# Performance work log

Measured on AMD Instinct MI355X. Metric: run time of the kernel, lower is better.

Reference implementation:

```python
import jax, jax.numpy as jnp
import numpy as np

B, L, DIM, H = 1, 2048, 3072, 24
D = DIM // H  # 128
EPS = 1e-6

def setup_inputs() -> dict:
    key = jax.random.key(0)
    ks = jax.random.split(key, 7)
    x = jax.random.normal(ks[0], (B, L, DIM), dtype=jnp.float32)
    pe = jax.random.normal(ks[1], (B, 1, L, D // 2, 2, 2), dtype=jnp.float32)
    w_qkv = jax.random.normal(ks[2], (DIM, 3 * DIM), dtype=jnp.float32) / np.sqrt(DIM)
    q_scale = jnp.ones((D,), dtype=jnp.float32)
    k_scale = jnp.ones((D,), dtype=jnp.float32)
    w_proj = jax.random.normal(ks[3], (DIM, DIM), dtype=jnp.float32) / np.sqrt(DIM)
    b_proj = jnp.zeros((DIM,), dtype=jnp.float32)
    return {"x": x, "pe": pe, "w_qkv": w_qkv, "q_scale": q_scale,
            "k_scale": k_scale, "w_proj": w_proj, "b_proj": b_proj}

def _rmsnorm(t, scale):
    # flax nn.RMSNorm: t * rsqrt(mean(t^2, -1) + eps) * scale
    ms = jnp.mean(jnp.square(t), axis=-1, keepdims=True)
    return t * jax.lax.rsqrt(ms + EPS) * scale

def _apply_rope(xq, xk, pe):
    # xq/xk: [B,H,L,D]; pe: [B,1,L,D/2,2,2]
    xq_ = xq.reshape(*xq.shape[:-1], -1, 1, 2)
    xk_ = xk.reshape(*xk.shape[:-1], -1, 1, 2)
    xq_out = pe[..., 0] * xq_[..., 0] + pe[..., 1] * xq_[..., 1]
    xk_out = pe[..., 0] * xk_[..., 0] + pe[..., 1] * xk_[..., 1]
    return xq_out.reshape(xq.shape), xk_out.reshape(xk.shape)

def reference(x, pe, w_qkv, q_scale, k_scale, w_proj, b_proj):
    qkv = jnp.einsum('bld,de->ble', x, w_qkv)            # [B,L,3*DIM]
    qkv = qkv.reshape(B, L, 3, H, D)
    qkv = jnp.moveaxis(qkv, 2, 0)                          # [3,B,H?,..]
    q, k, v = jnp.transpose(qkv, (0, 1, 3, 2, 4))          # each [B,H,L,D]
    q = _rmsnorm(q, q_scale).astype(v.dtype)
    k = _rmsnorm(k, k_scale).astype(v.dtype)
    q, k = _apply_rope(q, k, pe)
    scale = 1.0 / np.sqrt(D)
    scores = jnp.einsum('bhqd,bhkd->bhqk', q, k) * scale   # [B,H,L,L]
    attn = jax.nn.softmax(scores, axis=-1)
    out = jnp.einsum('bhqk,bhkd->bhqd', attn, v)           # [B,H,L,D]
    out = jnp.transpose(out, (0, 2, 1, 3)).reshape(B, L, DIM)
    return jnp.einsum('bld,de->ble', out, w_proj) + b_proj
```

## Files before the change

kernel.cpp:

```cpp
#include <hip/hip_runtime.h>

#define L_    2048
#define DIM_  3072
#define H_    24
#define D_    128
#define NQKV  9216

typedef __attribute__((ext_vector_type(8))) short bf16x8;
typedef __attribute__((ext_vector_type(4))) short bf16x4;
typedef __attribute__((ext_vector_type(4))) float f32x4;

__device__ __forceinline__ unsigned short f2bf(float f) {
  union { float f; unsigned u; } v; v.f = f;
  unsigned r = v.u + 0x7fffu + ((v.u >> 16) & 1u);
  return (unsigned short)(r >> 16);
}

__device__ __forceinline__ void gload_lds16(const void* g, void* l) {
  auto* lp = reinterpret_cast<__attribute__((address_space(3))) unsigned int*>(
      reinterpret_cast<uintptr_t>(l));
  auto* gp = reinterpret_cast<const __attribute__((address_space(1))) unsigned int*>(
      reinterpret_cast<uintptr_t>(g));
  __builtin_amdgcn_global_load_lds(gp, lp, 16, 0, 0);
}

__global__ __launch_bounds__(256)
void castAll(const float* __restrict__ x,  unsigned short* __restrict__ xb,
             const float* __restrict__ w0, unsigned short* __restrict__ o0,
             const float* __restrict__ w1, unsigned short* __restrict__ o1) {
  const int K = 3072;
  const int by = blockIdx.y;
  if (by >= 192) {
    int blk = (by - 192) * 24 + blockIdx.x;
    int total = (L_ * DIM_) >> 2;
    int stride = 2304 * 256;
    for (int i = blk * 256 + threadIdx.x; i < total; i += stride) {
      float4 v = ((const float4*)x)[i];
      ushort4 o;
      o.x = f2bf(v.x); o.y = f2bf(v.y); o.z = f2bf(v.z); o.w = f2bf(v.w);
      ((ushort4*)xb)[i] = o;
    }
    return;
  }
  const float* in; unsigned short* out; int N, n0;
  if (by < 144) { in = w0; out = o0; N = 9216; n0 = by * 64; }
  else          { in = w1; out = o1; N = 3072; n0 = (by - 144) * 64; }
  const int tid  = threadIdx.x;
  const int lane = tid & 63;
  const int wave = tid >> 6;
  const int nq = lane & 7;
  const int kq = lane >> 3;
  const int k0 = blockIdx.x * 128 + (wave & 1) * 64 + kq * 8;
  const int nb = n0 + (wave >> 1) * 32 + nq * 4;
  float4 v[8];
  #pragma unroll
  for (int i = 0; i < 8; i++)
    v[i] = *(const float4*)&in[(size_t)(k0 + i) * N + nb];
  #pragma unroll
  for (int j = 0; j < 4; j++) {
    bf16x8 o;
    #pragma unroll
    for (int i = 0; i < 8; i++)
      o[i] = (short)f2bf(((const float*)&v[i])[j]);
    *(bf16x8*)&out[(size_t)(nb + j) * K + k0] = o;
  }
}

__global__ __launch_bounds__(256, 3)
void gemm_qkv(const unsigned short* __restrict__ A,
              const unsigned short* __restrict__ Bt,
              const float* __restrict__ pe,
              const float* __restrict__ q_scale,
              const float* __restrict__ k_scale,
              unsigned short* __restrict__ Qo,
              unsigned short* __restrict__ Ko,
              unsigned short* __restrict__ Vt)
{
  const int K = DIM_;
  __shared__ __align__(16) unsigned short S[128 * 132];
  unsigned short* As = S;
  unsigned short* Bs = S + 128 * 64;
  const int tid  = threadIdx.x;
  const int wave = tid >> 6;
  const int lane = tid & 63;
  const int l15  = lane & 15;
  const int quad = lane >> 4;
  const int wm = wave >> 1, wn = wave & 1;

  const int lin = blockIdx.x;
  const int st  = lin >> 6;
  const int w6  = lin & 63;
  const int bn_idx = (st >> 1) * 8 + (w6 & 7);
  const int bm_idx = (st & 1) * 8 + (w6 >> 3);
  const int bm = bm_idx * 128;
  const int bn = bn_idx * 128;

  const int srow = lane >> 3;
  const int scol = (lane & 7) ^ srow;
  const unsigned short* Ag = A  + (size_t)(bm + wave * 32 + srow) * K + scol * 8;
  const unsigned short* Bg = Bt + (size_t)(bn + wave * 32 + srow) * K + scol * 8;
  unsigned short* Al = &As[(wave * 32) * 64];
  unsigned short* Bl = &Bs[(wave * 32) * 64];

  f32x4 acc[4][4];
  #pragma unroll
  for (int i = 0; i < 4; i++)
    #pragma unroll
    for (int j = 0; j < 4; j++) acc[i][j] = (f32x4){0.f, 0.f, 0.f, 0.f};

  for (int k0 = 0; k0 < K; k0 += 64) {
    __syncthreads();
    #pragma unroll
    for (int j = 0; j < 4; j++) {
      gload_lds16(Ag + (size_t)j * 8 * K + k0, Al + j * 8 * 64);
      gload_lds16(Bg + (size_t)j * 8 * K + k0, Bl + j * 8 * 64);
    }
    __syncthreads();
    #pragma unroll
    for (int ks = 0; ks < 2; ks++) {
      const int cph = ((ks * 4 + quad) ^ (l15 & 7)) * 8;
      bf16x8 af[4], bf[4];
      #pragma unroll
      for (int mt = 0; mt < 4; mt++)
        af[mt] = *(const bf16x8*)&As[(wm * 64 + mt * 16 + l15) * 64 + cph];
      #pragma unroll
      for (int nt = 0; nt < 4; nt++)
        bf[nt] = *(const bf16x8*)&Bs[(wn * 64 + nt * 16 + l15) * 64 + cph];
      #pragma unroll
      for (int mt = 0; mt < 4; mt++)
        #pragma unroll
        for (int nt = 0; nt < 4; nt++)
          acc[mt][nt] = __builtin_amdgcn_mfma_f32_16x16x32_bf16(
              af[mt], bf[nt], acc[mt][nt], 0, 0, 0);
    }
  }
  __syncthreads();

  if (bn_idx < 48) {
    const bool isQ = bn_idx < 24;
    const int  hh  = isQ ? bn_idx : bn_idx - 24;
    const float* sc = isQ ? q_scale : k_scale;
    unsigned short* dst = isQ ? Qo : Ko;
    float* rbuf = (float*)S;
    #pragma unroll
    for (int mt = 0; mt < 4; mt++)
      #pragma unroll
      for (int r = 0; r < 4; r++) {
        float p = 0.f;
        #pragma unroll
        for (int nt = 0; nt < 4; nt++) p += acc[mt][nt][r] * acc[mt][nt][r];
        p += __shfl_xor(p, 1); p += __shfl_xor(p, 2);
        p += __shfl_xor(p, 4); p += __shfl_xor(p, 8);
        if (l15 == 0) rbuf[wn * 128 + wm * 64 + mt * 16 + quad * 4 + r] = p;
      }
    __syncthreads();
    #pragma unroll
    for (int mt = 0; mt < 4; mt++)
      #pragma unroll
      for (int r = 0; r < 4; r++) {
        const int lrow = wm * 64 + mt * 16 + quad * 4 + r;
        const int lg = bm + lrow;
        float ms = (rbuf[lrow] + rbuf[128 + lrow]) * (1.f / 128.f);
        float rinv = rsqrtf(ms + 1e-6f);
        #pragma unroll
        for (int nt = 0; nt < 4; nt++) {
          const int d = wn * 64 + nt * 16 + l15;
          float n  = acc[mt][nt][r] * rinv * sc[d];
          float np = __shfl_xor(n, 1);
          float2 ab = *(const float2*)&pe[(size_t)lg * 256 + (d >> 1) * 4 + (d & 1) * 2];
          float xe = (d & 1) ? np : n;
          float xo = (d & 1) ? n  : np;
          float o = ab.x * xe + ab.y * xo;
          if (isQ) o *= (0.08838834764831845f * 1.4426950408889634f);
          dst[((size_t)hh * L_ + lg) * D_ + d] = f2bf(o);
        }
      }
  } else {
    const int hh = bn_idx - 48;
    unsigned short (*St)[132] = (unsigned short(*)[132])S;
    #pragma unroll
    for (int mt = 0; mt < 4; mt++)
      #pragma unroll
      for (int nt = 0; nt < 4; nt++)
        #pragma unroll
        for (int r = 0; r < 4; r++) {
          int row = wm * 64 + mt * 16 + quad * 4 + r;
          int col = wn * 64 + nt * 16 + l15;
          St[row][col] = f2bf(acc[mt][nt][r]);
        }
    __syncthreads();
    const int grp = tid >> 6;
    const int ll  = tid & 63;
    unsigned short* dstV = Vt + (size_t)hh * D_ * L_;
    #pragma unroll
    for (int dd = 0; dd < 32; dd += 4) {
      const int d = grp * 32 + dd;
      #pragma unroll
      for (int half = 0; half < 2; half++) {
        const int l = ll + half * 64;
        bf16x4 v4 = *(const bf16x4*)&St[l][d];
        #pragma unroll
        for (int j = 0; j < 4; j++)
          dstV[(size_t)(d + j) * L_ + bm + l] = ((const unsigned short*)&v4)[j];
      }
    }
  }
}

__global__ __launch_bounds__(256, 3)
void gemm_proj(const unsigned short* __restrict__ A,
               const unsigned short* __restrict__ Bt,
               const float* __restrict__ bias,
               float* __restrict__ out,
               int M, int N, int K)
{
  __shared__ unsigned short As[128 * 64];
  __shared__ unsigned short Bs[128 * 64];
  const int tid  = threadIdx.x;
  const int wave = tid >> 6;
  const int lane = tid & 63;
  const int l15  = lane & 15;
  const int quad = lane >> 4;
  const int wm = wave >> 1, wn = wave & 1;
  const int lin = blockIdx.x;
  const int st  = lin >> 6;
  const int w6  = lin & 63;
  const int bn = ((st >> 1) * 8 + (w6 & 7)) * 128;
  const int bm = ((st & 1) * 8 + (w6 >> 3)) * 128;

  const int srow = lane >> 3;
  const int scol = (lane & 7) ^ srow;
  const unsigned short* Ag = A  + (size_t)(bm + wave * 32 + srow) * K + scol * 8;
  const unsigned short* Bg = Bt + (size_t)(bn + wave * 32 + srow) * K + scol * 8;
  unsigned short* Al = &As[(wave * 32) * 64];
  unsigned short* Bl = &Bs[(wave * 32) * 64];

  f32x4 acc[4][4];
  #pragma unroll
  for (int i = 0; i < 4; i++)
    #pragma unroll
    for (int j = 0; j < 4; j++) acc[i][j] = (f32x4){0.f, 0.f, 0.f, 0.f};

  for (int k0 = 0; k0 < K; k0 += 64) {
    __syncthreads();
    #pragma unroll
    for (int j = 0; j < 4; j++) {
      gload_lds16(Ag + (size_t)j * 8 * K + k0, Al + j * 8 * 64);
      gload_lds16(Bg + (size_t)j * 8 * K + k0, Bl + j * 8 * 64);
    }
    __syncthreads();
    #pragma unroll
    for (int ks = 0; ks < 2; ks++) {
      const int cph = ((ks * 4 + quad) ^ (l15 & 7)) * 8;
      bf16x8 af[4], bf[4];
      #pragma unroll
      for (int mt = 0; mt < 4; mt++)
        af[mt] = *(const bf16x8*)&As[(wm * 64 + mt * 16 + l15) * 64 + cph];
      #pragma unroll
      for (int nt = 0; nt < 4; nt++)
        bf[nt] = *(const bf16x8*)&Bs[(wn * 64 + nt * 16 + l15) * 64 + cph];
      #pragma unroll
      for (int mt = 0; mt < 4; mt++)
        #pragma unroll
        for (int nt = 0; nt < 4; nt++)
          acc[mt][nt] = __builtin_amdgcn_mfma_f32_16x16x32_bf16(
              af[mt], bf[nt], acc[mt][nt], 0, 0, 0);
    }
  }
  float bcol[4];
  #pragma unroll
  for (int nt = 0; nt < 4; nt++)
    bcol[nt] = bias[bn + wn * 64 + nt * 16 + l15];
  #pragma unroll
  for (int mt = 0; mt < 4; mt++)
    #pragma unroll
    for (int nt = 0; nt < 4; nt++)
      #pragma unroll
      for (int r = 0; r < 4; r++) {
        int row = bm + wm * 64 + mt * 16 + quad * 4 + r;
        int col = bn + wn * 64 + nt * 16 + l15;
        out[(size_t)row * N + col] = acc[mt][nt][r] + bcol[nt];
      }
}

__global__ __launch_bounds__(256, 3)
void flash_attn(const unsigned short* __restrict__ Q,
                const unsigned short* __restrict__ K,
                const unsigned short* __restrict__ Vt,
                unsigned short* __restrict__ Out)
{
  __shared__ __align__(16) char smem[49152];
  float*  Obuf = (float*)smem;
  float2* mlb  = (float2*)(smem + 32768);
  float4* sAr  = (float4*)(smem + 33280);

  const int tid  = threadIdx.x;
  const int wave = tid >> 6;
  const int lane = tid & 63;
  const int l15  = lane & 15;
  const int quad = lane >> 4;
  const int qg = wave >> 1;
  const int kh = wave & 1;
  const int id   = blockIdx.x;
  const int slot = id >> 3;
  const int h    = (id & 7) * 3 + slot % 3;
  const int q0   = (slot / 3) * 64 + qg * 32;

  const unsigned short* Qh = Q  + (size_t)h * L_ * D_;
  const unsigned short* Kh = K  + (size_t)h * L_ * D_;
  const unsigned short* Vh = Vt + (size_t)h * D_ * L_;

  bf16x8 qf[2][4];
  #pragma unroll
  for (int nt = 0; nt < 2; nt++)
    #pragma unroll
    for (int kc = 0; kc < 4; kc++)
      qf[nt][kc] = *(const bf16x8*)&Qh[(size_t)(q0 + nt * 16 + l15) * D_ + kc * 32 + quad * 8];

  f32x4 oacc[2][8];
  #pragma unroll
  for (int i = 0; i < 2; i++)
    #pragma unroll
    for (int j = 0; j < 8; j++) oacc[i][j] = (f32x4){0.f, 0.f, 0.f, 0.f};
  float m_i[2] = {-1e30f, -1e30f}, l_i[2] = {0.f, 0.f};

  const int kr_l = lane >> 4;
  const int vr_l = lane >> 3;
  const int vcl  = (lane & 7) ^ vr_l;

  auto stageK = [&](int t, int b) {
    unsigned short* Ksb = (unsigned short*)(smem + b * 16384);
    #pragma unroll
    for (int ji = 0; ji < 4; ji++) {
      int Rr = wave * 16 + ji * 4;
      int cl = l15 ^ ((Rr + kr_l) & 15);
      gload_lds16(&Kh[(size_t)(t + Rr + kr_l) * D_ + cl * 8], &Ksb[Rr * 128]);
    }
  };
  auto stageV = [&](int t) {
    unsigned short* Vsb = (unsigned short*)(smem + 32768);
    #pragma unroll
    for (int ji = 0; ji < 4; ji++) {
      int R2 = wave * 32 + ji * 8;
      gload_lds16(&Vh[(size_t)(R2 + vr_l) * L_ + t + vcl * 8], &Vsb[R2 * 64]);
    }
  };

  stageK(0, 0);
  stageV(0);

  for (int t = 0; t < L_; t += 64) {
    const int cur = (t >> 6) & 1;
    const bool more = (t + 64 < L_);

    asm volatile("s_waitcnt vmcnt(4)" ::: "memory");
    __builtin_amdgcn_s_barrier();
    if (more) stageK(t + 64, cur ^ 1);

    const unsigned short* Ksc = (const unsigned short*)(smem + cur * 16384);
    const unsigned short* Vsc = (const unsigned short*)(smem + 32768);

    f32x4 s[2][2];
    #pragma unroll
    for (int i = 0; i < 2; i++)
      #pragma unroll
      for (int j = 0; j < 2; j++) s[i][j] = (f32x4){0.f, 0.f, 0.f, 0.f};
    __builtin_amdgcn_s_setprio(1);
    #pragma unroll
    for (int mt = 0; mt < 2; mt++) {
      const int krow = kh * 32 + mt * 16 + l15;
      #pragma unroll
      for (int kc = 0; kc < 4; kc++) {
        bf16x8 kf = *(const bf16x8*)&Ksc[krow * 128 + (((kc * 4 + quad) ^ l15) * 8)];
        s[mt][0] = __builtin_amdgcn_mfma_f32_16x16x32_bf16(kf, qf[0][kc], s[mt][0], 0, 0, 0);
        s[mt][1] = __builtin_amdgcn_mfma_f32_16x16x32_bf16(kf, qf[1][kc], s[mt][1], 0, 0, 0);
      }
    }
    __builtin_amdgcn_s_setprio(0);

    float vmax[2];
    #pragma unroll
    for (int nt = 0; nt < 2; nt++) {
      float a = fmaxf(fmaxf(s[0][nt][0], s[0][nt][1]), s[0][nt][2]);
      a = fmaxf(fmaxf(a, s[0][nt][3]), s[1][nt][0]);
      a = fmaxf(fmaxf(a, s[1][nt][1]), s[1][nt][2]);
      a = fmaxf(a, s[1][nt][3]);
      a = fmaxf(a, __shfl_xor(a, 16));
      vmax[nt] = fmaxf(a, __shfl_xor(a, 32));
    }
    if (!__all((vmax[0] - m_i[0] <= 11.5415603f) && (vmax[1] - m_i[1] <= 11.5415603f))) {
      float alpha[2];
      #pragma unroll
      for (int nt = 0; nt < 2; nt++) {
        float mnew = fmaxf(m_i[nt], vmax[nt]);
        alpha[nt] = exp2f(m_i[nt] - mnew);
        m_i[nt] = mnew;
        l_i[nt] *= alpha[nt];
      }
      float ar[2][4];
      #pragma unroll
      for (int qt = 0; qt < 2; qt++)
        #pragma unroll
        for (int r = 0; r < 4; r++)
          ar[qt][r] = __shfl(alpha[qt], quad * 4 + r);
      #pragma unroll
      for (int qt = 0; qt < 2; qt++)
        #pragma unroll
        for (int ntd = 0; ntd < 8; ntd++)
          #pragma unroll
          for (int r = 0; r < 4; r++)
            oacc[qt][ntd][r] *= ar[qt][r];
    }
    float rs[2] = {0.f, 0.f};
    #pragma unroll
    for (int mt = 0; mt < 2; mt++)
      #pragma unroll
      for (int nt = 0; nt < 2; nt++)
        #pragma unroll
        for (int r = 0; r < 4; r++) {
          float p = exp2f(s[mt][nt][r] - m_i[nt]);
          s[mt][nt][r] = p;
          rs[nt] += p;
        }
    #pragma unroll
    for (int nt = 0; nt < 2; nt++) {
      rs[nt] += __shfl_xor(rs[nt], 16);
      rs[nt] += __shfl_xor(rs[nt], 32);
      l_i[nt] += rs[nt];
    }
    bf16x4 pk[2][2];
    #pragma unroll
    for (int mt = 0; mt < 2; mt++)
      #pragma unroll
      for (int qt = 0; qt < 2; qt++) {
        union { unsigned int u2[2]; bf16x4 v4; } pku;
        asm("v_cvt_pk_bf16_f32 %0, %1, %2"
            : "=v"(pku.u2[0]) : "v"(s[mt][qt][0]), "v"(s[mt][qt][1]));
        asm("v_cvt_pk_bf16_f32 %0, %1, %2"
            : "=v"(pku.u2[1]) : "v"(s[mt][qt][2]), "v"(s[mt][qt][3]));
        pk[mt][qt] = pku.v4;
      }

    if (more) asm volatile("s_waitcnt vmcnt(4)" ::: "memory");
    else      asm volatile("s_waitcnt vmcnt(0)" ::: "memory");
    __builtin_amdgcn_s_barrier();

    __builtin_amdgcn_s_setprio(1);
    #pragma unroll
    for (int ntd = 0; ntd < 8; ntd++) {
      const int vrow = ntd * 16 + l15;
      #pragma unroll
      for (int mt = 0; mt < 2; mt++) {
        int phys = (kh * 4 + mt * 2 + (quad >> 1)) ^ (l15 & 7);
        bf16x4 vf = *(const bf16x4*)&Vsc[vrow * 64 + phys * 8 + (quad & 1) * 4];
        oacc[0][ntd] = __builtin_amdgcn_mfma_f32_16x16x16bf16_1k(pk[mt][0], vf, oacc[0][ntd], 0, 0, 0);
        oacc[1][ntd] = __builtin_amdgcn_mfma_f32_16x16x16bf16_1k(pk[mt][1], vf, oacc[1][ntd], 0, 0, 0);
      }
    }
    __builtin_amdgcn_s_setprio(0);

    if (more) {
      __builtin_amdgcn_s_barrier();
      stageV(t + 64);
    }
  }

  __syncthreads();
  if (kh == 1) {
    #pragma unroll
    for (int qt = 0; qt < 2; qt++)
      #pragma unroll
      for (int ntd = 0; ntd < 8; ntd++)
        #pragma unroll
        for (int r = 0; r < 4; r++)
          Obuf[(size_t)(qg * 32 + qt * 16 + quad * 4 + r) * 128 + ntd * 16 + l15] = oacc[qt][ntd][r];
    if (quad == 0)
      #pragma unroll
      for (int qt = 0; qt < 2; qt++)
        mlb[qg * 32 + qt * 16 + l15] = make_float2(m_i[qt], l_i[qt]);
  }
  __syncthreads();
  if (kh == 0 && quad == 0) {
    #pragma unroll
    for (int qt = 0; qt < 2; qt++) {
      float2 m1 = mlb[qg * 32 + qt * 16 + l15];
      float M  = fmaxf(m_i[qt], m1.x);
      float a0 = exp2f(m_i[qt] - M);
      float a1 = exp2f(m1.x - M);
      float Ls = l_i[qt] * a0 + m1.y * a1;
      sAr[qg * 32 + qt * 16 + l15] = make_float4(a0, a1, 1.f / Ls, 0.f);
    }
  }
  __syncthreads();
  if (kh == 0) {
    #pragma unroll
    for (int qt = 0; qt < 2; qt++)
      #pragma unroll
      for (int r = 0; r < 4; r++) {
        float4 A = sAr[qg * 32 + qt * 16 + quad * 4 + r];
        #pragma unroll
        for (int ntd = 0; ntd < 8; ntd++) {
          float o1 = Obuf[(size_t)(qg * 32 + qt * 16 + quad * 4 + r) * 128 + ntd * 16 + l15];
          float v  = (oacc[qt][ntd][r] * A.x + o1 * A.y) * A.z;
          Out[(size_t)(q0 + qt * 16 + quad * 4 + r) * DIM_ + h * D_ + ntd * 16 + l15] = f2bf(v);
        }
      }
  }
}

extern "C" void kernel_launch(void* const* d_in, const int* in_sizes, int n_in,
                              void* d_out, int out_size, void* d_ws, size_t ws_size,
                              hipStream_t stream) {
  const float* x       = (const float*)d_in[0];
  const float* pe      = (const float*)d_in[1];
  const float* w_qkv   = (const float*)d_in[2];
  const float* q_scale = (const float*)d_in[3];
  const float* k_scale = (const float*)d_in[4];
  const float* w_proj  = (const float*)d_in[5];
  const float* b_proj  = (const float*)d_in[6];

  unsigned short* w_qkvT  = (unsigned short*)d_ws;
  unsigned short* w_projT = w_qkvT + 28311552;
  unsigned short* x_b     = w_projT + 9437184;
  unsigned short* q_r     = x_b + 6291456;
  unsigned short* k_r     = q_r + 6291456;
  unsigned short* vt_r    = k_r + 6291456;
  unsigned short* attn_b  = vt_r + 6291456;

  castAll<<<dim3(24, 288), 256, 0, stream>>>(
      x, x_b, w_qkv, w_qkvT, w_proj, w_projT);

  gemm_qkv<<<1152, 256, 0, stream>>>(
      x_b, w_qkvT, pe, q_scale, k_scale, q_r, k_r, vt_r);

  flash_attn<<<768, 256, 0, stream>>>(q_r, k_r, vt_r, attn_b);

  gemm_proj<<<384, 256, 0, stream>>>(
      attn_b, w_projT, b_proj, (float*)d_out, 2048, 3072, 3072);
}
```

Measured before the change: 502.9 us.

## Rewrite flash attention with 32x32x16 MFMA, 2-wave blocks and no KV split

Flash attention now uses 128-thread blocks in which each wave owns 32 query rows and walks the full key sequence in 32-key tiles. Scores and PV products use the 32x32x16 bf16 MFMA, and the P fragment is rearranged with cross-half lane shuffles. The earlier split of keys across two waves, with its LDS-based merge of partial outputs, is removed, along with its extra syncs and shared memory. This gives fewer waves per block and less latency hiding in exchange for a smaller LDS footprint and a simpler epilogue.

```diff
diff --git a/kernel.cpp b/kernel.cpp
--- a/kernel.cpp
+++ b/kernel.cpp
@@ -9,6 +9,7 @@
 typedef __attribute__((ext_vector_type(8))) short bf16x8;
 typedef __attribute__((ext_vector_type(4))) short bf16x4;
 typedef __attribute__((ext_vector_type(4))) float f32x4;
+typedef __attribute__((ext_vector_type(16))) float f32x16;
 
 __device__ __forceinline__ unsigned short f2bf(float f) {
   union { float f; unsigned u; } v; v.f = f;
@@ -283,163 +284,138 @@
       }
 }
 
-__global__ __launch_bounds__(256, 3)
+__global__ __launch_bounds__(128, 3)
 void flash_attn(const unsigned short* __restrict__ Q,
                 const unsigned short* __restrict__ K,
                 const unsigned short* __restrict__ Vt,
                 unsigned short* __restrict__ Out)
 {
-  __shared__ __align__(16) char smem[49152];
-  float*  Obuf = (float*)smem;
-  float2* mlb  = (float2*)(smem + 32768);
-  float4* sAr  = (float4*)(smem + 33280);
+  __shared__ __align__(16) char smem[24576];
 
   const int tid  = threadIdx.x;
   const int wave = tid >> 6;
   const int lane = tid & 63;
-  const int l15  = lane & 15;
-  const int quad = lane >> 4;
-  const int qg = wave >> 1;
-  const int kh = wave & 1;
+  const int l31  = lane & 31;
+  const int h5   = lane >> 5;
   const int id   = blockIdx.x;
   const int slot = id >> 3;
   const int h    = (id & 7) * 3 + slot % 3;
-  const int q0   = (slot / 3) * 64 + qg * 32;
+  const int q0w  = (slot / 3) * 64 + wave * 32;
 
   const unsigned short* Qh = Q  + (size_t)h * L_ * D_;
   const unsigned short* Kh = K  + (size_t)h * L_ * D_;
   const unsigned short* Vh = Vt + (size_t)h * D_ * L_;
 
-  bf16x8 qf[2][4];
-  #pragma unroll
-  for (int nt = 0; nt < 2; nt++)
-    #pragma unroll
-    for (int kc = 0; kc < 4; kc++)
-      qf[nt][kc] = *(const bf16x8*)&Qh[(size_t)(q0 + nt * 16 + l15) * D_ + kc * 32 + quad * 8];
-
-  f32x4 oacc[2][8];
-  #pragma unroll
-  for (int i = 0; i < 2; i++)
-    #pragma unroll
-    for (int j = 0; j < 8; j++) oacc[i][j] = (f32x4){0.f, 0.f, 0.f, 0.f};
-  float m_i[2] = {-1e30f, -1e30f}, l_i[2] = {0.f, 0.f};
-
-  const int kr_l = lane >> 4;
-  const int vr_l = lane >> 3;
-  const int vcl  = (lane & 7) ^ vr_l;
+  bf16x8 qf[8];
+  #pragma unroll
+  for (int kc = 0; kc < 8; kc++)
+    qf[kc] = *(const bf16x8*)&Qh[(size_t)(q0w + l31) * D_ + kc * 16 + h5 * 8];
+
+  f32x16 oacc[4];
+  #pragma unroll
+  for (int i = 0; i < 4; i++)
+    #pragma unroll
+    for (int r = 0; r < 16; r++) oacc[i][r] = 0.f;
+  float m_i = -1e30f, l_i = 0.f;
 
   auto stageK = [&](int t, int b) {
-    unsigned short* Ksb = (unsigned short*)(smem + b * 16384);
-    #pragma unroll
-    for (int ji = 0; ji < 4; ji++) {
-      int Rr = wave * 16 + ji * 4;
-      int cl = l15 ^ ((Rr + kr_l) & 15);
-      gload_lds16(&Kh[(size_t)(t + Rr + kr_l) * D_ + cl * 8], &Ksb[Rr * 128]);
+    unsigned short* Kb = (unsigned short*)(smem + b * 8192);
+    #pragma unroll
+    for (int j = 0; j < 4; j++) {
+      int R0 = wave * 16 + j * 4;
+      int R  = R0 + (lane >> 4);
+      gload_lds16(&Kh[(size_t)(t + R) * D_ + (((lane & 15) ^ (R & 15)) * 8)],
+                  &Kb[R0 * 128]);
     }
   };
   auto stageV = [&](int t) {
-    unsigned short* Vsb = (unsigned short*)(smem + 32768);
-    #pragma unroll
-    for (int ji = 0; ji < 4; ji++) {
-      int R2 = wave * 32 + ji * 8;
-      gload_lds16(&Vh[(size_t)(R2 + vr_l) * L_ + t + vcl * 8], &Vsb[R2 * 64]);
+    unsigned short* Vb = (unsigned short*)(smem + 16384);
+    #pragma unroll
+    for (int j = 0; j < 4; j++) {
+      int R0 = wave * 64 + j * 16;
+      int R  = R0 + (lane >> 2);
+      gload_lds16(&Vh[(size_t)R * L_ + t + (((lane & 3) ^ (R & 3)) * 8)],
+                  &Vb[R0 * 32]);
     }
   };
 
   stageK(0, 0);
   stageV(0);
 
-  for (int t = 0; t < L_; t += 64) {
-    const int cur = (t >> 6) & 1;
-    const bool more = (t + 64 < L_);
+  for (int t = 0; t < L_; t += 32) {
+    const int cur  = (t >> 5) & 1;
+    const bool more = (t + 32 < L_);
 
     asm volatile("s_waitcnt vmcnt(4)" ::: "memory");
     __builtin_amdgcn_s_barrier();
-    if (more) stageK(t + 64, cur ^ 1);
-
-    const unsigned short* Ksc = (const unsigned short*)(smem + cur * 16384);
-    const unsigned short* Vsc = (const unsigned short*)(smem + 32768);
-
-    f32x4 s[2][2];
-    #pragma unroll
-    for (int i = 0; i < 2; i++)
-      #pragma unroll
-      for (int j = 0; j < 2; j++) s[i][j] = (f32x4){0.f, 0.f, 0.f, 0.f};
+    if (more) stageK(t + 32, cur ^ 1);
+
+    const unsigned short* Ksc = (const unsigned short*)(smem + cur * 8192);
+    const unsigned short* Vsc = (const unsigned short*)(smem + 16384);
+
+    f32x16 s;
+    #pragma unroll
+    for (int r = 0; r < 16; r++) s[r] = 0.f;
     __builtin_amdgcn_s_setprio(1);
     #pragma unroll
-    for (int mt = 0; mt < 2; mt++) {
-      const int krow = kh * 32 + mt * 16 + l15;
-      #pragma unroll
-      for (int kc = 0; kc < 4; kc++) {
-        bf16x8 kf = *(const bf16x8*)&Ksc[krow * 128 + (((kc * 4 + quad) ^ l15) * 8)];
-        s[mt][0] = __builtin_amdgcn_mfma_f32_16x16x32_bf16(kf, qf[0][kc], s[mt][0], 0, 0, 0);
-        s[mt][1] = __builtin_amdgcn_mfma_f32_16x16x32_bf16(kf, qf[1][kc], s[mt][1], 0, 0, 0);
-      }
+    for (int kc = 0; kc < 8; kc++) {
+      bf16x8 kf = *(const bf16x8*)
+          &Ksc[l31 * 128 + (((kc * 2 + h5) ^ (lane & 15)) * 8)];
+      s = __builtin_amdgcn_mfma_f32_32x32x16_bf16(kf, qf[kc], s, 0, 0, 0);
     }
     __builtin_amdgcn_s_setprio(0);
 
-    float vmax[2];
-    #pragma unroll
-    for (int nt = 0; nt < 2; nt++) {
-      float a = fmaxf(fmaxf(s[0][nt][0], s[0][nt][1]), s[0][nt][2]);
-      a = fmaxf(fmaxf(a, s[0][nt][3]), s[1][nt][0]);
-      a = fmaxf(fmaxf(a, s[1][nt][1]), s[1][nt][2]);
-      a = fmaxf(a, s[1][nt][3]);
-      a = fmaxf(a, __shfl_xor(a, 16));
-      vmax[nt] = fmaxf(a, __shfl_xor(a, 32));
-    }
-    if (!__all((vmax[0] - m_i[0] <= 11.5415603f) && (vmax[1] - m_i[1] <= 11.5415603f))) {
-      float alpha[2];
-      #pragma unroll
-      for (int nt = 0; nt < 2; nt++) {
-        float mnew = fmaxf(m_i[nt], vmax[nt]);
-        alpha[nt] = exp2f(m_i[nt] - mnew);
-        m_i[nt] = mnew;
-        l_i[nt] *= alpha[nt];
-      }
-      float ar[2][4];
-      #pragma unroll
-      for (int qt = 0; qt < 2; qt++)
-        #pragma unroll
-        for (int r = 0; r < 4; r++)
-          ar[qt][r] = __shfl(alpha[qt], quad * 4 + r);
-      #pragma unroll
-      for (int qt = 0; qt < 2; qt++)
-        #pragma unroll
-        for (int ntd = 0; ntd < 8; ntd++)
-          #pragma unroll
-          for (int r = 0; r < 4; r++)
-            oacc[qt][ntd][r] *= ar[qt][r];
-    }
-    float rs[2] = {0.f, 0.f};
-    #pragma unroll
-    for (int mt = 0; mt < 2; mt++)
-      #pragma unroll
-      for (int nt = 0; nt < 2; nt++)
-        #pragma unroll
-        for (int r = 0; r < 4; r++) {
-          float p = exp2f(s[mt][nt][r] - m_i[nt]);
-          s[mt][nt][r] = p;
-          rs[nt] += p;
-        }
-    #pragma unroll
-    for (int nt = 0; nt < 2; nt++) {
-      rs[nt] += __shfl_xor(rs[nt], 16);
-      rs[nt] += __shfl_xor(rs[nt], 32);
-      l_i[nt] += rs[nt];
-    }
-    bf16x4 pk[2][2];
-    #pragma unroll
-    for (int mt = 0; mt < 2; mt++)
-      #pragma unroll
-      for (int qt = 0; qt < 2; qt++) {
-        union { unsigned int u2[2]; bf16x4 v4; } pku;
-        asm("v_cvt_pk_bf16_f32 %0, %1, %2"
-            : "=v"(pku.u2[0]) : "v"(s[mt][qt][0]), "v"(s[mt][qt][1]));
-        asm("v_cvt_pk_bf16_f32 %0, %1, %2"
-            : "=v"(pku.u2[1]) : "v"(s[mt][qt][2]), "v"(s[mt][qt][3]));
-        pk[mt][qt] = pku.v4;
-      }
+    float a0 = fmaxf(fmaxf(s[0], s[1]), s[2]);
+    a0 = fmaxf(fmaxf(a0, s[3]), s[4]);
+    a0 = fmaxf(fmaxf(a0, s[5]), s[6]);
+    a0 = fmaxf(fmaxf(a0, s[7]), s[8]);
+    a0 = fmaxf(fmaxf(a0, s[9]), s[10]);
+    a0 = fmaxf(fmaxf(a0, s[11]), s[12]);
+    a0 = fmaxf(fmaxf(a0, s[13]), s[14]);
+    a0 = fmaxf(a0, s[15]);
+    float vmax = fmaxf(a0, __shfl_xor(a0, 32));
+    if (!__all(vmax - m_i <= 11.5415603f)) {
+      float mnew = fmaxf(m_i, vmax);
+      float alpha = exp2f(m_i - mnew);
+      m_i = mnew;
+      l_i *= alpha;
+      #pragma unroll
+      for (int db = 0; db < 4; db++)
+        #pragma unroll
+        for (int r = 0; r < 16; r++) oacc[db][r] *= alpha;
+    }
+    float rs = 0.f;
+    #pragma unroll
+    for (int r = 0; r < 16; r++) {
+      float p = exp2f(s[r] - m_i);
+      s[r] = p;
+      rs += p;
+    }
+    rs += __shfl_xor(rs, 32);
+    l_i += rs;
+
+    unsigned int w[8];
+    #pragma unroll
+    for (int j = 0; j < 8; j++)
+      asm("v_cvt_pk_bf16_f32 %0, %1, %2"
+          : "=v"(w[j]) : "v"(s[2 * j]), "v"(s[2 * j + 1]));
+
+    bf16x8 pb[2];
+    #pragma unroll
+    for (int ks = 0; ks < 2; ks++) {
+      unsigned int keep0 = h5 ? w[4 * ks + 2] : w[4 * ks];
+      unsigned int keep1 = h5 ? w[4 * ks + 3] : w[4 * ks + 1];
+      unsigned int send0 = h5 ? w[4 * ks]     : w[4 * ks + 2];
+      unsigned int send1 = h5 ? w[4 * ks + 1] : w[4 * ks + 3];
+      unsigned int recv0 = __shfl_xor((int)send0, 32);
+      unsigned int recv1 = __shfl_xor((int)send1, 32);
+      union { unsigned int u[4]; bf16x8 v; } fb;
+      fb.u[0] = h5 ? recv0 : keep0;
+      fb.u[1] = h5 ? recv1 : keep1;
+      fb.u[2] = h5 ? keep0 : recv0;
+      fb.u[3] = h5 ? keep1 : recv1;
+      pb[ks] = fb.v;
+    }
 
     if (more) asm volatile("s_waitcnt vmcnt(4)" ::: "memory");
     else      asm volatile("s_waitcnt vmcnt(0)" ::: "memory");
@@ -447,65 +423,35 @@
 
     __builtin_amdgcn_s_setprio(1);
     #pragma unroll
-    for (int ntd = 0; ntd < 8; ntd++) {
-      const int vrow = ntd * 16 + l15;
-      #pragma unroll
-      for (int mt = 0; mt < 2; mt++) {
-        int phys = (kh * 4 + mt * 2 + (quad >> 1)) ^ (l15 & 7);
-        bf16x4 vf = *(const bf16x4*)&Vsc[vrow * 64 + phys * 8 + (quad & 1) * 4];
-        oacc[0][ntd] = __builtin_amdgcn_mfma_f32_16x16x16bf16_1k(pk[mt][0], vf, oacc[0][ntd], 0, 0, 0);
-        oacc[1][ntd] = __builtin_amdgcn_mfma_f32_16x16x16bf16_1k(pk[mt][1], vf, oacc[1][ntd], 0, 0, 0);
+    for (int db = 0; db < 4; db++) {
+      #pragma unroll
+      for (int ks = 0; ks < 2; ks++) {
+        bf16x8 vf = *(const bf16x8*)
+            &Vsc[(db * 32 + l31) * 32 + (((ks * 2 + h5) ^ (lane & 3)) * 8)];
+        oacc[db] = __builtin_amdgcn_mfma_f32_32x32x16_bf16(vf, pb[ks], oacc[db], 0, 0, 0);
       }
     }
     __builtin_amdgcn_s_setprio(0);
 
     if (more) {
       __builtin_amdgcn_s_barrier();
-      stageV(t + 64);
-    }
-  }
-
-  __syncthreads();
-  if (kh == 1) {
-    #pragma unroll
-    for (int qt = 0; qt < 2; qt++)
-      #pragma unroll
-      for (int ntd = 0; ntd < 8; ntd++)
-        #pragma unroll
-        for (int r = 0; r < 4; r++)
-          Obuf[(size_t)(qg * 32 + qt * 16 + quad * 4 + r) * 128 + ntd * 16 + l15] = oacc[qt][ntd][r];
-    if (quad == 0)
-      #pragma unroll
-      for (int qt = 0; qt < 2; qt++)
-        mlb[qg * 32 + qt * 16 + l15] = make_float2(m_i[qt], l_i[qt]);
-  }
-  __syncthreads();
-  if (kh == 0 && quad == 0) {
-    #pragma unroll
-    for (int qt = 0; qt < 2; qt++) {
-      float2 m1 = mlb[qg * 32 + qt * 16 + l15];
-      float M  = fmaxf(m_i[qt], m1.x);
-      float a0 = exp2f(m_i[qt] - M);
-      float a1 = exp2f(m1.x - M);
-      float Ls = l_i[qt] * a0 + m1.y * a1;
-      sAr[qg * 32 + qt * 16 + l15] = make_float4(a0, a1, 1.f / Ls, 0.f);
-    }
-  }
-  __syncthreads();
-  if (kh == 0) {
-    #pragma unroll
-    for (int qt = 0; qt < 2; qt++)
-      #pragma unroll
-      for (int r = 0; r < 4; r++) {
-        float4 A = sAr[qg * 32 + qt * 16 + quad * 4 + r];
-        #pragma unroll
-        for (int ntd = 0; ntd < 8; ntd++) {
-          float o1 = Obuf[(size_t)(qg * 32 + qt * 16 + quad * 4 + r) * 128 + ntd * 16 + l15];
-          float v  = (oacc[qt][ntd][r] * A.x + o1 * A.y) * A.z;
-          Out[(size_t)(q0 + qt * 16 + quad * 4 + r) * DIM_ + h * D_ + ntd * 16 + l15] = f2bf(v);
-        }
-      }
-  }
+      stageV(t + 32);
+    }
+  }
+
+  float rinv = 1.f / l_i;
+  const size_t obase = (size_t)(q0w + l31) * DIM_ + h * D_;
+  #pragma unroll
+  for (int db = 0; db < 4; db++)
+    #pragma unroll
+    for (int j = 0; j < 4; j++) {
+      ushort4 o;
+      o.x = f2bf(oacc[db][4 * j + 0] * rinv);
+      o.y = f2bf(oacc[db][4 * j + 1] * rinv);
+      o.z = f2bf(oacc[db][4 * j + 2] * rinv);
+      o.w = f2bf(oacc[db][4 * j + 3] * rinv);
+      *(ushort4*)&Out[obase + db * 32 + 8 * j + 4 * h5] = o;
+    }
 }
 
 extern "C" void kernel_launch(void* const* d_in, const int* in_sizes, int n_in,
@@ -533,7 +479,7 @@
   gemm_qkv<<<1152, 256, 0, stream>>>(
       x_b, w_qkvT, pe, q_scale, k_scale, q_r, k_r, vt_r);
 
-  flash_attn<<<768, 256, 0, stream>>>(q_r, k_r, vt_r, attn_b);
+  flash_attn<<<768, 128, 0, stream>>>(q_r, k_r, vt_r, attn_b);
 
   gemm_proj<<<384, 256, 0, stream>>>(
       attn_b, w_projT, b_proj, (float*)d_out, 2048, 3072, 3072);
```

New measurement: 520.8 us. +3.6%, slower.
